# Performance work log

Hardware: AMD Instinct MI355X
Metric: run time of the kernel (lower is better)

Reference implementation:

```python
import jax, jax.numpy as jnp
import numpy as np

B, D, T = 8, 256, 4096      # batch, latent dim, frames
NQ, K = 8, 1024             # num quantizers, codebook size


def setup_inputs() -> dict:
    key = jax.random.key(0)
    k1, k2 = jax.random.split(key)
    x = jax.random.normal(k1, (B, D, T), dtype=jnp.float32)
    codebooks = jax.random.normal(k2, (NQ, K, D), dtype=jnp.float32)
    return {"x": x, "codebooks": codebooks}


def _vq(residual, cb):
    """Single VQ stage: nearest-neighbor in cb, lookup, VQ loss.
    residual: [B, T, D], cb: [K, D]
    """
    sg = jax.lax.stop_gradient
    dots = jnp.einsum('btd,kd->btk', residual, cb)                 # [B,T,K]
    dist = (residual ** 2).sum(-1, keepdims=True) - 2.0 * dots + (cb ** 2).sum(-1)
    idx = jnp.argmin(dist, axis=-1)                                # [B,T]
    q = cb[idx]                                                    # gather [B,T,D]
    # commitment loss + codebook loss (standard VQ-VAE combination)
    loss = jnp.mean((sg(q) - residual) ** 2) + jnp.mean((q - sg(residual)) ** 2)
    return q, idx, loss


def reference(x, codebooks):
    """Residual VQ forward (eval mode, train=False).
    x: [B, D, T]; codebooks: [NQ, K, D]
    Returns (quantized_out [B,T,D], indices [NQ,B,T], losses [NQ]).
    """
    residual0 = jnp.transpose(x, (0, 2, 1))                        # [B,T,D]

    def step(carry, cb):
        res, qout = carry
        q, idx, loss = _vq(res, cb)
        q = jax.lax.stop_gradient(q)
        return (res - q, qout + q), (idx, loss)

    (_, quantized_out), (indices, losses) = jax.lax.scan(
        step, (residual0, jnp.zeros_like(residual0)), codebooks)
    return quantized_out, indices, losses
```

## Files before the change

kernel.cpp:

```cpp
#include <hip/hip_runtime.h>

#define B_   8
#define D_   256
#define T_   4096
#define NQ_  8
#define K_   1024

#define IDX_OFF  ((size_t)B_ * T_ * D_)
#define LOSS_OFF (IDX_OFF + (size_t)NQ_ * B_ * T_)

#define XT_OFF   0ull
#define CB16_OFF 33554432ull
#define CN_OFF   37748736ull
#define LB_OFF   37781504ull

typedef _Float16 half8 __attribute__((ext_vector_type(8)));
typedef float   f32x16 __attribute__((ext_vector_type(16)));

__device__ __forceinline__ ushort f2h(float f) {
  return __builtin_bit_cast(ushort, (_Float16)f);
}

__device__ __forceinline__ float packsc(float sc, uint code) {
  return __builtin_bit_cast(float, (__builtin_bit_cast(uint, sc) & ~1023u) | code);
}
__device__ __forceinline__ void ins3(float& v1, float& v2, float& v3, float f) {
  const float a = v1;
  const float m = fmaxf(v1, f);
  v1 = fminf(v1, f);
  const float v2n = __builtin_amdgcn_fmed3f(a, v2, f);
  v3 = __builtin_amdgcn_fmed3f(v2, v3, m);
  v2 = v2n;
}

__global__ void prep_xT(const float* __restrict__ x, float* __restrict__ xT) {
  __shared__ float tile[64][65];
  const int bidx = blockIdx.x;
  const int b = bidx >> 8, dc = (bidx >> 6) & 3, tc = bidx & 63;
  const int d0 = dc * 64, t0 = tc * 64;
  const int tid = threadIdx.x;
  {
    const int tt = tid & 63, dg = tid >> 6;
    for (int i = 0; i < 16; ++i) {
      const int d = dg * 16 + i;
      tile[d][tt] = x[((size_t)(b * D_ + d0 + d)) * T_ + t0 + tt];
    }
  }
  __syncthreads();
  {
    const int dw = tid & 63, tg = tid >> 6;
    for (int i = 0; i < 16; ++i) {
      const int t = tg * 16 + i;
      xT[((size_t)b * T_ + t0 + t) * D_ + d0 + dw] = tile[dw][t];
    }
  }
}

__global__ void prep_cb16(const float* __restrict__ cb, ushort* __restrict__ cb16,
                          float* __restrict__ cnorm) {
  const int tid = threadIdx.x, w = tid >> 6, l = tid & 63;
  const int code = blockIdx.x * 4 + w;
  const int s = code >> 10, ci = code & 1023, tile = ci >> 5, n = ci & 31;
  const float* row = cb + (size_t)code * D_;
  const float4 v = *(const float4*)(row + l * 4);
  double nrm = (double)v.x * v.x + (double)v.y * v.y + (double)v.z * v.z + (double)v.w * v.w;
  ushort4 p;
  p.x = f2h(v.x); p.y = f2h(v.y); p.z = f2h(v.z); p.w = f2h(v.w);
  const int ks = l >> 2, lf = ((l >> 1) & 1) * 32 + n, j0 = (l & 1) * 4;
  const size_t off = (((size_t)s * 32 + tile) * 16 + ks) * 512 + (size_t)lf * 8 + j0;
  *(ushort4*)(cb16 + off) = p;
#pragma unroll
  for (int m = 1; m <= 32; m <<= 1) nrm += __shfl_xor(nrm, m);
  if (l == 0) cnorm[code] = (float)nrm;
}

__global__ __launch_bounds__(256)
void rvq_main(const float* __restrict__ cb, const float* __restrict__ xT,
              const ushort* __restrict__ cb16, const float* __restrict__ cnorm,
              float* __restrict__ out, double* __restrict__ lossbuf) {
  __shared__ __align__(16) uint4  res16[2048];
  __shared__ float candm[64][12];
  __shared__ double lred[4];

  const int tid = threadIdx.x;
  const int w = tid >> 6, l = tid & 63, n5 = l & 31, h = l >> 5;
  const size_t row0 = (size_t)blockIdx.x * 64;
  const int rowL31 = tid >> 3;
  const int dq = tid & 7;

  float res[2][4][8];

#pragma unroll
  for (int g3 = 0; g3 < 2; ++g3) {
#pragma unroll
    for (int cc = 0; cc < 4; ++cc) {
      const int kb = dq * 4 + cc;
      const float* xp = xT + (row0 + g3 * 32 + rowL31) * D_ + kb * 8;
      const float4 x0 = *(const float4*)xp, x1 = *(const float4*)(xp + 4);
      res[g3][cc][0] = x0.x; res[g3][cc][1] = x0.y; res[g3][cc][2] = x0.z; res[g3][cc][3] = x0.w;
      res[g3][cc][4] = x1.x; res[g3][cc][5] = x1.y; res[g3][cc][6] = x1.z; res[g3][cc][7] = x1.w;
      uint4 pv;
      pv.x = __builtin_bit_cast(uint, __builtin_amdgcn_cvt_pkrtz(x0.x, x0.y));
      pv.y = __builtin_bit_cast(uint, __builtin_amdgcn_cvt_pkrtz(x0.z, x0.w));
      pv.z = __builtin_bit_cast(uint, __builtin_amdgcn_cvt_pkrtz(x1.x, x1.y));
      pv.w = __builtin_bit_cast(uint, __builtin_amdgcn_cvt_pkrtz(x1.z, x1.w));
      res16[g3 * 1024 + kb * 32 + (rowL31 ^ dq)] = pv;
    }
  }
  __syncthreads();

  for (int s = 0; s < NQ_; ++s) {
    float a1v = 3e38f, a2v = 3e38f, a3v = 3e38f;
    float b1v = 3e38f, b2v = 3e38f, b3v = 3e38f;
    float c1v = 3e38f, c2v = 3e38f, c3v = 3e38f;
    float d1v = 3e38f, d2v = 3e38f, d3v = 3e38f;
    for (int tt = 0; tt < 8; ++tt) {
      const int t = w * 8 + tt;
      const uint4* ap = (const uint4*)(cb16 + ((size_t)(s * 32 + t) * 16) * 512) + l;
      int zr = 0;
      asm volatile("" : "+v"(zr));
      const uint4* bp = res16 + zr;
      f32x16 acc0, acc1;
#pragma unroll
      for (int r = 0; r < 16; ++r) { acc0[r] = 0.0f; acc1[r] = 0.0f; }
#pragma unroll
      for (int q = 0; q < 4; ++q) {
        uint4 av[4], b0[4], b1[4];
#pragma unroll
        for (int c = 0; c < 4; ++c) {
          const int ks = q * 4 + c;
          const int bo = (ks * 2 + h) * 32 + (n5 ^ ((ks >> 1) & 7));
          av[c] = ap[(size_t)ks * 64];
          b0[c] = bp[bo];
          b1[c] = bp[1024 + bo];
        }
#pragma unroll
        for (int c = 0; c < 4; ++c) {
          acc0 = __builtin_amdgcn_mfma_f32_32x32x16_f16(
              __builtin_bit_cast(half8, av[c]), __builtin_bit_cast(half8, b0[c]), acc0, 0, 0, 0);
          acc1 = __builtin_amdgcn_mfma_f32_32x32x16_f16(
              __builtin_bit_cast(half8, av[c]), __builtin_bit_cast(half8, b1[c]), acc1, 0, 0, 0);
        }
      }
      const float* cnb = cnorm + s * K_ + t * 32 + h * 4;
      const uint cbase = (uint)(t * 32 + 4 * h);
#pragma unroll
      for (int qq = 0; qq < 4; ++qq) {
        const float4 cq = *(const float4*)(cnb + qq * 8);
        const float cna[4] = {cq.x, cq.y, cq.z, cq.w};
#pragma unroll
        for (int rr = 0; rr < 4; ++rr) {
          const int r = qq * 4 + rr;
          const uint code = cbase + (uint)(8 * qq + rr);
          const float f0 = packsc(fmaf(-2.0f, acc0[r], cna[rr]), code);
          const float f1 = packsc(fmaf(-2.0f, acc1[r], cna[rr]), code);
          if (rr & 1) { ins3(b1v, b2v, b3v, f0); ins3(d1v, d2v, d3v, f1); }
          else        { ins3(a1v, a2v, a3v, f0); ins3(c1v, c2v, c3v, f1); }
        }
      }
    }
    ins3(a1v, a2v, a3v, b1v); ins3(a1v, a2v, a3v, b2v); ins3(a1v, a2v, a3v, b3v);
    ins3(c1v, c2v, c3v, d1v); ins3(c1v, c2v, c3v, d2v); ins3(c1v, c2v, c3v, d3v);
    {
      const float o1 = __shfl_xor(a1v, 32), o2 = __shfl_xor(a2v, 32), o3 = __shfl_xor(a3v, 32);
      ins3(a1v, a2v, a3v, o1); ins3(a1v, a2v, a3v, o2); ins3(a1v, a2v, a3v, o3);
      const float p1 = __shfl_xor(c1v, 32), p2 = __shfl_xor(c2v, 32), p3 = __shfl_xor(c3v, 32);
      ins3(c1v, c2v, c3v, p1); ins3(c1v, c2v, c3v, p2); ins3(c1v, c2v, c3v, p3);
    }
    if (h == 0) {
      candm[n5][w * 3 + 0] = a1v; candm[n5][w * 3 + 1] = a2v; candm[n5][w * 3 + 2] = a3v;
      candm[32 + n5][w * 3 + 0] = c1v; candm[32 + n5][w * 3 + 1] = c2v; candm[32 + n5][w * 3 + 2] = c3v;
    }
    __syncthreads();

    double lossW = 0.0;
#pragma unroll
    for (int g3 = 0; g3 < 2; ++g3) {
      const int row = g3 * 32 + rowL31;
      float m1 = 3e38f, m2 = 3e38f, m3 = 3e38f;
#pragma unroll
      for (int cd = 0; cd < 12; ++cd) ins3(m1, m2, m3, candm[row][cd]);
      const int c1 = (int)(__builtin_bit_cast(uint, m1) & 1023u);
      const int c2 = (int)(__builtin_bit_cast(uint, m2) & 1023u);
      const int c3 = (int)(__builtin_bit_cast(uint, m3) & 1023u);

      const float* cbs = cb + (size_t)s * K_ * D_;
      const float* cr0 = cbs + (size_t)c1 * D_;
      const float* cr1 = cbs + (size_t)c2 * D_;
      const float* cr2 = cbs + (size_t)c3 * D_;
      double dd0 = 0.0, dd1 = 0.0, dd2 = 0.0;
#pragma unroll
      for (int cc = 0; cc < 4; ++cc) {
        const int kb = dq * 4 + cc;
        const int go = kb * 8;
        const float4 a0 = *(const float4*)(cr0 + go), a1 = *(const float4*)(cr0 + go + 4);
        const float4 b0 = *(const float4*)(cr1 + go), b1 = *(const float4*)(cr1 + go + 4);
        const float4 g0 = *(const float4*)(cr2 + go), g1 = *(const float4*)(cr2 + go + 4);
        const float af[8] = {a0.x, a0.y, a0.z, a0.w, a1.x, a1.y, a1.z, a1.w};
        const float bf[8] = {b0.x, b0.y, b0.z, b0.w, b1.x, b1.y, b1.z, b1.w};
        const float gf[8] = {g0.x, g0.y, g0.z, g0.w, g1.x, g1.y, g1.z, g1.w};
#pragma unroll
        for (int j = 0; j < 8; ++j) {
          const double r64 = (double)res[g3][cc][j];
          const double u = r64 - (double)af[j]; dd0 += u * u;
          const double v = r64 - (double)bf[j]; dd1 += v * v;
          const double gg = r64 - (double)gf[j]; dd2 += gg * gg;
        }
      }
#pragma unroll
      for (int m = 1; m <= 4; m <<= 1) {
        dd0 += __shfl_xor(dd0, m); dd1 += __shfl_xor(dd1, m); dd2 += __shfl_xor(dd2, m);
      }
      int win = c1; double dwn = dd0;
      if (dd1 < dwn || (dd1 == dwn && c2 < win)) { win = c2; dwn = dd1; }
      if (dd2 < dwn || (dd2 == dwn && c3 < win)) { win = c3; dwn = dd2; }
      const float* crw = cbs + (size_t)win * D_;
#pragma unroll
      for (int cc = 0; cc < 4; ++cc) {
        const int kb = dq * 4 + cc;
        const int go = kb * 8;
        const float4 w0 = *(const float4*)(crw + go), w1 = *(const float4*)(crw + go + 4);
        const float wf[8] = {w0.x, w0.y, w0.z, w0.w, w1.x, w1.y, w1.z, w1.w};
        if (s < NQ_ - 1) {
#pragma unroll
          for (int j = 0; j < 8; ++j) res[g3][cc][j] = res[g3][cc][j] - wf[j];
          uint4 pv;
          pv.x = __builtin_bit_cast(uint, __builtin_amdgcn_cvt_pkrtz(res[g3][cc][0], res[g3][cc][1]));
          pv.y = __builtin_bit_cast(uint, __builtin_amdgcn_cvt_pkrtz(res[g3][cc][2], res[g3][cc][3]));
          pv.z = __builtin_bit_cast(uint, __builtin_amdgcn_cvt_pkrtz(res[g3][cc][4], res[g3][cc][5]));
          pv.w = __builtin_bit_cast(uint, __builtin_amdgcn_cvt_pkrtz(res[g3][cc][6], res[g3][cc][7]));
          res16[g3 * 1024 + kb * 32 + (rowL31 ^ dq)] = pv;
        } else {
          const float* xp = xT + (row0 + row) * D_ + go;
          const float4 x0 = *(const float4*)xp, x1 = *(const float4*)(xp + 4);
          const float xf[8] = {x0.x, x0.y, x0.z, x0.w, x1.x, x1.y, x1.z, x1.w};
          float o[8];
#pragma unroll
          for (int j = 0; j < 8; ++j) o[j] = xf[j] - (res[g3][cc][j] - wf[j]);
          float* od = out + (row0 + row) * D_ + go;
          *(float4*)od       = make_float4(o[0], o[1], o[2], o[3]);
          *(float4*)(od + 4) = make_float4(o[4], o[5], o[6], o[7]);
        }
      }
      if (dq == 0) {
        out[IDX_OFF + (size_t)s * (B_ * T_) + row0 + row] = (float)win;
        lossW += dwn;
      }
    }
#pragma unroll
    for (int m = 8; m <= 32; m <<= 1) lossW += __shfl_xor(lossW, m);
    if (l == 0) lred[w] = lossW;
    __syncthreads();
    if (tid == 0)
      lossbuf[(size_t)s * 512 + blockIdx.x] = lred[0] + lred[1] + lred[2] + lred[3];
  }
}

__global__ void rvq_loss(const double* __restrict__ lossbuf, float* __restrict__ out) {
  const int s = blockIdx.x, tid = threadIdx.x;
  double acc = lossbuf[(size_t)s * 512 + tid] + lossbuf[(size_t)s * 512 + tid + 256];
#pragma unroll
  for (int m = 1; m <= 32; m <<= 1) acc += __shfl_xor(acc, m);
  __shared__ double sred[4];
  if ((tid & 63) == 0) sred[tid >> 6] = acc;
  __syncthreads();
  if (tid == 0)
    out[LOSS_OFF + s] =
        (float)(2.0 * (sred[0] + sred[1] + sred[2] + sred[3]) / (double)((size_t)B_ * T_ * D_));
}

extern "C" void kernel_launch(void* const* d_in, const int* in_sizes, int n_in,
                              void* d_out, int out_size, void* d_ws, size_t ws_size,
                              hipStream_t stream) {
  const float* x  = (const float*)d_in[0];
  const float* cb = (const float*)d_in[1];
  float* out = (float*)d_out;
  char* ws = (char*)d_ws;
  float*  xTp   = (float*)(ws + XT_OFF);
  ushort* cb16p = (ushort*)(ws + CB16_OFF);
  float*  cnp   = (float*)(ws + CN_OFF);
  double* lbp   = (double*)(ws + LB_OFF);

  prep_xT<<<2048, 256, 0, stream>>>(x, xTp);
  prep_cb16<<<2048, 256, 0, stream>>>(cb, cb16p, cnp);
  rvq_main<<<512, 256, 0, stream>>>(cb, xTp, cb16p, cnp, out, lbp);
  rvq_loss<<<8, 256, 0, stream>>>(lbp, out);
}
```

Measured before the change: 490.3 us.

## Double-buffer codebook tiles into LDS via async global_load_lds

Instead of loading fp16 codebook fragments straight from global memory into registers, each wave now streams them through a per-wave two-slot LDS buffer with global_load_lds. The next chunk is prefetched while MFMAs run on the current one, with manual vmcnt waits. The tile loop is flattened and fully unrolled, and the codebook-norm loads are hoisted to the start of each tile. The aim is to hide global load latency, at the cost of extra LDS and reliance on hand-written waitcnt counts, with no explicit barrier between the async LDS write and the read.

```diff
diff --git a/kernel.cpp b/kernel.cpp
--- a/kernel.cpp
+++ b/kernel.cpp
@@ -31,6 +31,18 @@
   const float v2n = __builtin_amdgcn_fmed3f(a, v2, f);
   v3 = __builtin_amdgcn_fmed3f(v2, v3, m);
   v2 = v2n;
+}
+
+__device__ __forceinline__ void stage_chunk(const uint4* ap0, uint4* aslotw, int slot, int i) {
+  const int t_ = i >> 2, q_ = i & 3;
+#pragma unroll
+  for (int c = 0; c < 4; ++c) {
+    const uint4* g = ap0 + (size_t)t_ * 1024 + (size_t)(q_ * 4 + c) * 64;
+    __builtin_amdgcn_global_load_lds(
+        (const __attribute__((address_space(1))) void*)g,
+        (__attribute__((address_space(3))) void*)(aslotw + slot * 256 + c * 64),
+        16, 0, 0);
+  }
 }
 
 __global__ void prep_xT(const float* __restrict__ x, float* __restrict__ xT) {
@@ -79,6 +91,7 @@
               const ushort* __restrict__ cb16, const float* __restrict__ cnorm,
               float* __restrict__ out, double* __restrict__ lossbuf) {
   __shared__ __align__(16) uint4  res16[2048];
+  __shared__ __align__(16) uint4  aslot[4][2][256];
   __shared__ float candm[64][12];
   __shared__ double lred[4];
 
@@ -110,52 +123,69 @@
   __syncthreads();
 
   for (int s = 0; s < NQ_; ++s) {
+    const uint4* ap0 = (const uint4*)(cb16 + ((size_t)(s * 32 + w * 8) * 16) * 512) + l;
+    uint4* aslotw = &aslot[w][0][0];
+    stage_chunk(ap0, aslotw, 0, 0);
+
     float a1v = 3e38f, a2v = 3e38f, a3v = 3e38f;
     float b1v = 3e38f, b2v = 3e38f, b3v = 3e38f;
     float c1v = 3e38f, c2v = 3e38f, c3v = 3e38f;
     float d1v = 3e38f, d2v = 3e38f, d3v = 3e38f;
-    for (int tt = 0; tt < 8; ++tt) {
-      const int t = w * 8 + tt;
-      const uint4* ap = (const uint4*)(cb16 + ((size_t)(s * 32 + t) * 16) * 512) + l;
-      int zr = 0;
-      asm volatile("" : "+v"(zr));
-      const uint4* bp = res16 + zr;
-      f32x16 acc0, acc1;
-#pragma unroll
-      for (int r = 0; r < 16; ++r) { acc0[r] = 0.0f; acc1[r] = 0.0f; }
-#pragma unroll
-      for (int q = 0; q < 4; ++q) {
-        uint4 av[4], b0[4], b1[4];
-#pragma unroll
-        for (int c = 0; c < 4; ++c) {
-          const int ks = q * 4 + c;
-          const int bo = (ks * 2 + h) * 32 + (n5 ^ ((ks >> 1) & 7));
-          av[c] = ap[(size_t)ks * 64];
-          b0[c] = bp[bo];
-          b1[c] = bp[1024 + bo];
-        }
-#pragma unroll
-        for (int c = 0; c < 4; ++c) {
-          acc0 = __builtin_amdgcn_mfma_f32_32x32x16_f16(
-              __builtin_bit_cast(half8, av[c]), __builtin_bit_cast(half8, b0[c]), acc0, 0, 0, 0);
-          acc1 = __builtin_amdgcn_mfma_f32_32x32x16_f16(
-              __builtin_bit_cast(half8, av[c]), __builtin_bit_cast(half8, b1[c]), acc1, 0, 0, 0);
-        }
-      }
-      const float* cnb = cnorm + s * K_ + t * 32 + h * 4;
-      const uint cbase = (uint)(t * 32 + 4 * h);
-#pragma unroll
-      for (int qq = 0; qq < 4; ++qq) {
-        const float4 cq = *(const float4*)(cnb + qq * 8);
-        const float cna[4] = {cq.x, cq.y, cq.z, cq.w};
-#pragma unroll
-        for (int rr = 0; rr < 4; ++rr) {
-          const int r = qq * 4 + rr;
-          const uint code = cbase + (uint)(8 * qq + rr);
-          const float f0 = packsc(fmaf(-2.0f, acc0[r], cna[rr]), code);
-          const float f1 = packsc(fmaf(-2.0f, acc1[r], cna[rr]), code);
-          if (rr & 1) { ins3(b1v, b2v, b3v, f0); ins3(d1v, d2v, d3v, f1); }
-          else        { ins3(a1v, a2v, a3v, f0); ins3(c1v, c2v, c3v, f1); }
+    int zr = 0;
+    asm volatile("" : "+v"(zr));
+    const uint4* bp = res16 + zr;
+    f32x16 acc0, acc1;
+    float4 cq[4];
+
+#pragma unroll
+    for (int i = 0; i < 32; ++i) {
+      const int tt = i >> 2, q = i & 3, sl = i & 1;
+      if (q == 0) {
+        const float* cnb = cnorm + s * K_ + (w * 8 + tt) * 32 + h * 4;
+        cq[0] = *(const float4*)(cnb);
+        cq[1] = *(const float4*)(cnb + 8);
+        cq[2] = *(const float4*)(cnb + 16);
+        cq[3] = *(const float4*)(cnb + 24);
+#pragma unroll
+        for (int r = 0; r < 16; ++r) { acc0[r] = 0.0f; acc1[r] = 0.0f; }
+      }
+      if (i + 1 < 32) {
+        stage_chunk(ap0, aslotw, (i + 1) & 1, i + 1);
+        asm volatile("s_waitcnt vmcnt(4)" ::: "memory");
+      } else {
+        asm volatile("s_waitcnt vmcnt(0)" ::: "memory");
+      }
+      uint4 av[4], b0[4], b1[4];
+#pragma unroll
+      for (int c = 0; c < 4; ++c) {
+        const int ks = q * 4 + c;
+        const int bo = (ks * 2 + h) * 32 + (n5 ^ ((ks >> 1) & 7));
+        av[c] = aslotw[sl * 256 + c * 64 + l];
+        b0[c] = bp[bo];
+        b1[c] = bp[1024 + bo];
+      }
+#pragma unroll
+      for (int c = 0; c < 4; ++c) {
+        acc0 = __builtin_amdgcn_mfma_f32_32x32x16_f16(
+            __builtin_bit_cast(half8, av[c]), __builtin_bit_cast(half8, b0[c]), acc0, 0, 0, 0);
+        acc1 = __builtin_amdgcn_mfma_f32_32x32x16_f16(
+            __builtin_bit_cast(half8, av[c]), __builtin_bit_cast(half8, b1[c]), acc1, 0, 0, 0);
+      }
+      if (q == 3) {
+        const int t = w * 8 + tt;
+        const uint cbase = (uint)(t * 32 + 4 * h);
+#pragma unroll
+        for (int qq = 0; qq < 4; ++qq) {
+          const float cna[4] = {cq[qq].x, cq[qq].y, cq[qq].z, cq[qq].w};
+#pragma unroll
+          for (int rr = 0; rr < 4; ++rr) {
+            const int r = qq * 4 + rr;
+            const uint code = cbase + (uint)(8 * qq + rr);
+            const float f0 = packsc(fmaf(-2.0f, acc0[r], cna[rr]), code);
+            const float f1 = packsc(fmaf(-2.0f, acc1[r], cna[rr]), code);
+            if (rr & 1) { ins3(b1v, b2v, b3v, f0); ins3(d1v, d2v, d3v, f1); }
+            else        { ins3(a1v, a2v, a3v, f0); ins3(c1v, c2v, c3v, f1); }
+          }
         }
       }
     }
```

New measurement: 517.3 us. +5.5%, slower.
